# Kernel optimization log

Measured on AMD Instinct MI355X. Metric: run time of the kernel, lower is better.

## Reference

```python
import jax, jax.numpy as jnp
import numpy as np

B, IN, H = 131072, 128, 128


def _linear_params(key, out_dim, in_dim):
    k1, k2 = jax.random.split(key)
    bound = 1.0 / np.sqrt(in_dim)
    W = jax.random.uniform(k1, (out_dim, in_dim), jnp.float32, -bound, bound)
    b = jax.random.uniform(k2, (out_dim,), jnp.float32, -bound, bound)
    return W, b


def setup_inputs() -> dict:
    key = jax.random.key(0)
    ks = jax.random.split(key, 11)
    X = jax.random.normal(ks[0], (B, IN), jnp.float32)
    h_prev = jax.random.normal(ks[1], (B, H), jnp.float32)
    c_prev = jax.random.normal(ks[2], (B, H), jnp.float32)
    names = ['xf', 'hf', 'xi', 'hi', 'xc', 'hc', 'xo', 'ho']
    params = {}
    for i, n in enumerate(names):
        in_dim = IN if n[0] == 'x' else H
        W, b = _linear_params(ks[3 + i], H, in_dim)
        params[f'W_{n}'] = W
        params[f'b_{n}'] = b
    return {'X': X, 'h_prev': h_prev, 'c_prev': c_prev, **params}


def reference(X, h_prev, c_prev,
              W_xf, b_xf, W_hf, b_hf,
              W_xi, b_xi, W_hi, b_hi,
              W_xc, b_xc, W_hc, b_hc,
              W_xo, b_xo, W_ho, b_ho):
    # Fuse the 8 small GEMMs into 2 concatenated GEMMs (x->4H, h->4H)
    Wx = jnp.concatenate([W_xf, W_xi, W_xc, W_xo], axis=0)  # [4H, IN]
    Wh = jnp.concatenate([W_hf, W_hi, W_hc, W_ho], axis=0)  # [4H, H]
    bx = jnp.concatenate([b_xf, b_xi, b_xc, b_xo])
    bh = jnp.concatenate([b_hf, b_hi, b_hc, b_ho])
    gates = X @ Wx.T + h_prev @ Wh.T + bx + bh  # [B, 4H]
    f, i, c_til, o = jnp.split(gates, 4, axis=-1)
    f_t = jax.nn.sigmoid(f)
    i_t = jax.nn.sigmoid(i)
    c_tilde_t = jnp.tanh(c_til)
    o_t = jax.nn.sigmoid(o)
    c_t = f_t * c_prev + i_t * c_tilde_t
    h_t = o_t * jnp.tanh(c_t)
    return (h_t, c_t)
```

## Files before the change

### kernel.cpp

```cpp
#include <hip/hip_runtime.h>
#include <hip/hip_bf16.h>

#define B_ROWS 131072
#define H 128
#define BM 32
#define TILES 8
#define NBLK (B_ROWS / (BM * TILES))

typedef __bf16 bf16x8 __attribute__((ext_vector_type(8)));
typedef float f32x4 __attribute__((ext_vector_type(4)));

#define LOG2E 1.4426950408889634f

__device__ __forceinline__ float fast_sigmoid(float x) {
    return __builtin_amdgcn_rcpf(1.0f + __builtin_amdgcn_exp2f(-LOG2E * x));
}
__device__ __forceinline__ float fast_tanh(float x) {
    return 1.0f - 2.0f * __builtin_amdgcn_rcpf(1.0f + __builtin_amdgcn_exp2f(2.0f * LOG2E * x));
}

struct WPtrs {
    const float* wx[4];
    const float* wh[4];
    const float* bx[4];
    const float* bh[4];
};

__global__ __launch_bounds__(256) void prep_weights(WPtrs p, __bf16* __restrict__ wcat,
                                                    float* __restrict__ bsum) {
    int n = blockIdx.x;
    int k = threadIdx.x;
    int g = n >> 7, r = n & 127;
    float v = (k < H) ? p.wx[g][r * H + k] : p.wh[g][r * H + (k - H)];
    wcat[n * 256 + k] = (__bf16)v;
    if (k == 0) bsum[n] = p.bx[g][r] + p.bh[g][r];
}

__global__ __launch_bounds__(512, 2) void lstm_fused(
    const float* __restrict__ X, const float* __restrict__ Hp, const float* __restrict__ Cp,
    const __bf16* __restrict__ Wcat, const float* __restrict__ Bsum,
    float* __restrict__ out)
{
    __shared__ char alds[BM * 512];

    const int t = threadIdx.x;
    const int lane = t & 63;
    const int cg = t >> 6;
    const int l16 = lane & 15;
    const int kg = lane >> 4;
    const long base = (long)blockIdx.x * (BM * TILES);
    const long c_off = (long)B_ROWS * H;

    const int j = cg * 16 + l16;
    const __bf16* wbase = Wcat + (long)j * 256 + kg * 8;

    float bias[4];
#pragma unroll
    for (int g = 0; g < 4; ++g) bias[g] = Bsum[g * H + j];

    const int r_q0 = t >> 5;
    const int r_q1 = 16 + (t >> 5);
    const int c4 = t & 31;

    float4 sx[2], sh[2];

    sx[0] = *(const float4*)(X  + (base + r_q0) * H + c4 * 4);
    sh[0] = *(const float4*)(Hp + (base + r_q0) * H + c4 * 4);
    sx[1] = *(const float4*)(X  + (base + r_q1) * H + c4 * 4);
    sh[1] = *(const float4*)(Hp + (base + r_q1) * H + c4 * 4);

    for (int tile = 0; tile < TILES; ++tile) {
        const long r0 = base + tile * BM;

#pragma unroll
        for (int q = 0; q < 2; ++q) {
            int row = q ? r_q1 : r_q0;
            int swz = (row & 7) << 4;
            union { __bf16 b[4]; unsigned long long u; } px, ph;
            float4 vx = sx[q], vh = sh[q];
            px.b[0] = (__bf16)vx.x; px.b[1] = (__bf16)vx.y;
            px.b[2] = (__bf16)vx.z; px.b[3] = (__bf16)vx.w;
            ph.b[0] = (__bf16)vh.x; ph.b[1] = (__bf16)vh.y;
            ph.b[2] = (__bf16)vh.z; ph.b[3] = (__bf16)vh.w;
            *(unsigned long long*)(alds + row * 512 + ((c4 * 8) ^ swz)) = px.u;
            *(unsigned long long*)(alds + row * 512 + ((256 + c4 * 8) ^ swz)) = ph.u;
        }
        __syncthreads();

        float cpv[8];
#pragma unroll
        for (int rt = 0; rt < 2; ++rt)
#pragma unroll
            for (int r = 0; r < 4; ++r)
                cpv[rt * 4 + r] = Cp[(r0 + rt * 16 + kg * 4 + r) * H + j];

        if (tile + 1 < TILES) {
            long rn = r0 + BM;
            sx[0] = *(const float4*)(X  + (rn + r_q0) * H + c4 * 4);
            sh[0] = *(const float4*)(Hp + (rn + r_q0) * H + c4 * 4);
            sx[1] = *(const float4*)(X  + (rn + r_q1) * H + c4 * 4);
            sh[1] = *(const float4*)(Hp + (rn + r_q1) * H + c4 * 4);
        }

        f32x4 acc[4][2] = {};
#pragma unroll
        for (int kc = 0; kc < 8; ++kc) {
            bf16x8 a[2];
#pragma unroll
            for (int rt = 0; rt < 2; ++rt) {
                int row = rt * 16 + l16;
                int off = row * 512 + ((kc * 64 + kg * 16) ^ ((row & 7) << 4));
                a[rt] = *(const bf16x8*)(alds + off);
            }
#pragma unroll
            for (int g = 0; g < 4; ++g) {
                bf16x8 b = *(const bf16x8*)(wbase + g * (128 * 256) + kc * 32);
                acc[g][0] = __builtin_amdgcn_mfma_f32_16x16x32_bf16(a[0], b, acc[g][0], 0, 0, 0);
                acc[g][1] = __builtin_amdgcn_mfma_f32_16x16x32_bf16(a[1], b, acc[g][1], 0, 0, 0);
            }
        }
        __syncthreads();

#pragma unroll
        for (int rt = 0; rt < 2; ++rt) {
#pragma unroll
            for (int r = 0; r < 4; ++r) {
                long row = r0 + rt * 16 + kg * 4 + r;
                float f  = acc[0][rt][r] + bias[0];
                float ii = acc[1][rt][r] + bias[1];
                float cl = acc[2][rt][r] + bias[2];
                float oo = acc[3][rt][r] + bias[3];
                float ft = fast_sigmoid(f);
                float it = fast_sigmoid(ii);
                float cc = fast_tanh(cl);
                float ot = fast_sigmoid(oo);
                float ct = ft * cpv[rt * 4 + r] + it * cc;
                float ht = ot * fast_tanh(ct);
                out[row * H + j] = ht;
                out[c_off + row * H + j] = ct;
            }
        }
    }
}

extern "C" void kernel_launch(void* const* d_in, const int* in_sizes, int n_in,
                              void* d_out, int out_size, void* d_ws, size_t ws_size,
                              hipStream_t stream) {
    const float* X  = (const float*)d_in[0];
    const float* Hp = (const float*)d_in[1];
    const float* Cp = (const float*)d_in[2];
    WPtrs p;
    p.wx[0] = (const float*)d_in[3];  p.bx[0] = (const float*)d_in[4];
    p.wh[0] = (const float*)d_in[5];  p.bh[0] = (const float*)d_in[6];
    p.wx[1] = (const float*)d_in[7];  p.bx[1] = (const float*)d_in[8];
    p.wh[1] = (const float*)d_in[9];  p.bh[1] = (const float*)d_in[10];
    p.wx[2] = (const float*)d_in[11]; p.bx[2] = (const float*)d_in[12];
    p.wh[2] = (const float*)d_in[13]; p.bh[2] = (const float*)d_in[14];
    p.wx[3] = (const float*)d_in[15]; p.bx[3] = (const float*)d_in[16];
    p.wh[3] = (const float*)d_in[17]; p.bh[3] = (const float*)d_in[18];

    __bf16* wcat = (__bf16*)d_ws;
    float*  bsum = (float*)((char*)d_ws + 512 * 256 * 2);

    prep_weights<<<512, 256, 0, stream>>>(p, wcat, bsum);
    lstm_fused<<<NBLK, 512, 0, stream>>>(X, Hp, Cp, wcat, bsum, (float*)d_out);
}
```

Baseline: 106.7 us.

## Load A fragments directly from global memory and drop LDS tiling loop

Removes shared-memory staging of X/h_prev and the per-block loop over 8 row tiles. Each block now processes a single 32-row tile, and each wave converts its MFMA A-fragments to bf16 straight from global loads. This avoids LDS writes, barriers and swizzle math, and gives more blocks for latency hiding. The cost is that every wave re-reads the same activation rows, relying on cache, and the software prefetch overlap and weight reuse across tiles are lost.

Result: slower. 262.2 us (+145.7%).

```diff
diff --git a/kernel.cpp b/kernel.cpp
--- a/kernel.cpp
+++ b/kernel.cpp
@@ -3,9 +3,6 @@
 
 #define B_ROWS 131072
 #define H 128
-#define BM 32
-#define TILES 8
-#define NBLK (B_ROWS / (BM * TILES))
 
 typedef __bf16 bf16x8 __attribute__((ext_vector_type(8)));
 typedef float f32x4 __attribute__((ext_vector_type(4)));
@@ -36,19 +33,17 @@
     if (k == 0) bsum[n] = p.bx[g][r] + p.bh[g][r];
 }
 
-__global__ __launch_bounds__(512, 2) void lstm_fused(
+__global__ __launch_bounds__(512) void lstm_fused(
     const float* __restrict__ X, const float* __restrict__ Hp, const float* __restrict__ Cp,
     const __bf16* __restrict__ Wcat, const float* __restrict__ Bsum,
     float* __restrict__ out)
 {
-    __shared__ char alds[BM * 512];
-
     const int t = threadIdx.x;
     const int lane = t & 63;
     const int cg = t >> 6;
     const int l16 = lane & 15;
     const int kg = lane >> 4;
-    const long base = (long)blockIdx.x * (BM * TILES);
+    const long r0 = (long)blockIdx.x * 32;
     const long c_off = (long)B_ROWS * H;
 
     const int j = cg * 16 + l16;
@@ -58,87 +53,62 @@
 #pragma unroll
     for (int g = 0; g < 4; ++g) bias[g] = Bsum[g * H + j];
 
-    const int r_q0 = t >> 5;
-    const int r_q1 = 16 + (t >> 5);
-    const int c4 = t & 31;
-
-    float4 sx[2], sh[2];
-
-    sx[0] = *(const float4*)(X  + (base + r_q0) * H + c4 * 4);
-    sh[0] = *(const float4*)(Hp + (base + r_q0) * H + c4 * 4);
-    sx[1] = *(const float4*)(X  + (base + r_q1) * H + c4 * 4);
-    sh[1] = *(const float4*)(Hp + (base + r_q1) * H + c4 * 4);
-
-    for (int tile = 0; tile < TILES; ++tile) {
-        const long r0 = base + tile * BM;
+    f32x4 acc[4][2] = {};
 
 #pragma unroll
-        for (int q = 0; q < 2; ++q) {
-            int row = q ? r_q1 : r_q0;
-            int swz = (row & 7) << 4;
-            union { __bf16 b[4]; unsigned long long u; } px, ph;
-            float4 vx = sx[q], vh = sh[q];
-            px.b[0] = (__bf16)vx.x; px.b[1] = (__bf16)vx.y;
-            px.b[2] = (__bf16)vx.z; px.b[3] = (__bf16)vx.w;
-            ph.b[0] = (__bf16)vh.x; ph.b[1] = (__bf16)vh.y;
-            ph.b[2] = (__bf16)vh.z; ph.b[3] = (__bf16)vh.w;
-            *(unsigned long long*)(alds + row * 512 + ((c4 * 8) ^ swz)) = px.u;
-            *(unsigned long long*)(alds + row * 512 + ((256 + c4 * 8) ^ swz)) = ph.u;
-        }
-        __syncthreads();
+    for (int kc = 0; kc < 8; ++kc) {
+        bf16x8 b[4];
+#pragma unroll
+        for (int g = 0; g < 4; ++g)
+            b[g] = *(const bf16x8*)(wbase + g * (128 * 256) + kc * 32);
 
-        float cpv[8];
+        bf16x8 a[2];
 #pragma unroll
-        for (int rt = 0; rt < 2; ++rt)
-#pragma unroll
-            for (int r = 0; r < 4; ++r)
-                cpv[rt * 4 + r] = Cp[(r0 + rt * 16 + kg * 4 + r) * H + j];
-
-        if (tile + 1 < TILES) {
-            long rn = r0 + BM;
-            sx[0] = *(const float4*)(X  + (rn + r_q0) * H + c4 * 4);
-            sh[0] = *(const float4*)(Hp + (rn + r_q0) * H + c4 * 4);
-            sx[1] = *(const float4*)(X  + (rn + r_q1) * H + c4 * 4);
-            sh[1] = *(const float4*)(Hp + (rn + r_q1) * H + c4 * 4);
+        for (int rt = 0; rt < 2; ++rt) {
+            long row = r0 + rt * 16 + l16;
+            const float* ap = (kc < 4 ? X + row * H + kc * 32
+                                      : Hp + row * H + (kc - 4) * 32) + kg * 8;
+            float4 lo = *(const float4*)ap;
+            float4 hi = *(const float4*)(ap + 4);
+            union { __bf16 e[8]; bf16x8 v; } u;
+            u.e[0] = (__bf16)lo.x; u.e[1] = (__bf16)lo.y;
+            u.e[2] = (__bf16)lo.z; u.e[3] = (__bf16)lo.w;
+            u.e[4] = (__bf16)hi.x; u.e[5] = (__bf16)hi.y;
+            u.e[6] = (__bf16)hi.z; u.e[7] = (__bf16)hi.w;
+            a[rt] = u.v;
         }
 
-        f32x4 acc[4][2] = {};
 #pragma unroll
-        for (int kc = 0; kc < 8; ++kc) {
-            bf16x8 a[2];
+        for (int g = 0; g < 4; ++g) {
+            acc[g][0] = __builtin_amdgcn_mfma_f32_16x16x32_bf16(a[0], b[g], acc[g][0], 0, 0, 0);
+            acc[g][1] = __builtin_amdgcn_mfma_f32_16x16x32_bf16(a[1], b[g], acc[g][1], 0, 0, 0);
+        }
+    }
+
+    float cpv[8];
 #pragma unroll
-            for (int rt = 0; rt < 2; ++rt) {
-                int row = rt * 16 + l16;
-                int off = row * 512 + ((kc * 64 + kg * 16) ^ ((row & 7) << 4));
-                a[rt] = *(const bf16x8*)(alds + off);
-            }
+    for (int rt = 0; rt < 2; ++rt)
 #pragma unroll
-            for (int g = 0; g < 4; ++g) {
-                bf16x8 b = *(const bf16x8*)(wbase + g * (128 * 256) + kc * 32);
-                acc[g][0] = __builtin_amdgcn_mfma_f32_16x16x32_bf16(a[0], b, acc[g][0], 0, 0, 0);
-                acc[g][1] = __builtin_amdgcn_mfma_f32_16x16x32_bf16(a[1], b, acc[g][1], 0, 0, 0);
-            }
-        }
-        __syncthreads();
+        for (int r = 0; r < 4; ++r)
+            cpv[rt * 4 + r] = Cp[(r0 + rt * 16 + kg * 4 + r) * H + j];
 
 #pragma unroll
-        for (int rt = 0; rt < 2; ++rt) {
+    for (int rt = 0; rt < 2; ++rt) {
 #pragma unroll
-            for (int r = 0; r < 4; ++r) {
-                long row = r0 + rt * 16 + kg * 4 + r;
-                float f  = acc[0][rt][r] + bias[0];
-                float ii = acc[1][rt][r] + bias[1];
-                float cl = acc[2][rt][r] + bias[2];
-                float oo = acc[3][rt][r] + bias[3];
-                float ft = fast_sigmoid(f);
-                float it = fast_sigmoid(ii);
-                float cc = fast_tanh(cl);
-                float ot = fast_sigmoid(oo);
-                float ct = ft * cpv[rt * 4 + r] + it * cc;
-                float ht = ot * fast_tanh(ct);
-                out[row * H + j] = ht;
-                out[c_off + row * H + j] = ct;
-            }
+        for (int r = 0; r < 4; ++r) {
+            long row = r0 + rt * 16 + kg * 4 + r;
+            float f  = acc[0][rt][r] + bias[0];
+            float ii = acc[1][rt][r] + bias[1];
+            float cl = acc[2][rt][r] + bias[2];
+            float oo = acc[3][rt][r] + bias[3];
+            float ft = fast_sigmoid(f);
+            float it = fast_sigmoid(ii);
+            float cc = fast_tanh(cl);
+            float ot = fast_sigmoid(oo);
+            float ct = ft * cpv[rt * 4 + r] + it * cc;
+            float ht = ot * fast_tanh(ct);
+            out[row * H + j] = ht;
+            out[c_off + row * H + j] = ct;
         }
     }
 }
@@ -163,5 +133,5 @@
     float*  bsum = (float*)((char*)d_ws + 512 * 256 * 2);
 
     prep_weights<<<512, 256, 0, stream>>>(p, wcat, bsum);
-    lstm_fused<<<NBLK, 512, 0, stream>>>(X, Hp, Cp, wcat, bsum, (float*)d_out);
+    lstm_fused<<<B_ROWS / 32, 512, 0, stream>>>(X, Hp, Cp, wcat, bsum, (float*)d_out);
 }
```
